# Optimization experiments

Hardware: AMD Instinct MI355X
Metric: run time of the kernel (lower is better)

## Reference

```python
import jax, jax.numpy as jnp
import numpy as np

B, T, N, F = 8, 64, 512, 64
H, FOUT = 128, 64
K = 3          # cheb_k
S = 3          # num_scales
EPS = 1e-8
SPARSITY = 0.3
TEMP = 1.0     # cheb_temp (buffer, temperature == 1.0)


def _xavier(key, fan_out, fan_in, gain):
    limit = gain * np.sqrt(6.0 / (fan_in + fan_out))
    return jax.random.uniform(key, (fan_out, fan_in), jnp.float32, -limit, limit)


def setup_inputs() -> dict:
    key = jax.random.key(0)
    ks = jax.random.split(key, 4)
    x = jax.random.normal(ks[0], (B, T, N, F), jnp.float32)
    # A_param: eye + 0.01*noise, symmetrized (improved_init, N > 64)
    A_param = jnp.eye(N, dtype=jnp.float32) + 0.01 * jax.random.normal(ks[1], (N, N), jnp.float32)
    A_param = 0.5 * (A_param + A_param.T)
    return {
        "x": x,
        "A_param": A_param,
        "alpha_logit": jnp.array(0.0, jnp.float32),  # logit(0.5)
        "in_w": _xavier(ks[2], H, F, np.sqrt(2.0)),
        "in_b": jnp.zeros((H,), jnp.float32),
        "out_w": _xavier(ks[3], FOUT, H, 1.0),
        "out_b": jnp.zeros((FOUT,), jnp.float32),
        "gn_in_w": jnp.ones((F,), jnp.float32), "gn_in_b": jnp.zeros((F,), jnp.float32), "gn_in_ms": jnp.ones((1,), jnp.float32),
        "gn_h_w": jnp.ones((H,), jnp.float32), "gn_h_b": jnp.zeros((H,), jnp.float32), "gn_h_ms": jnp.ones((1,), jnp.float32),
        "gn_out_w": jnp.ones((FOUT,), jnp.float32), "gn_out_b": jnp.zeros((FOUT,), jnp.float32), "gn_out_ms": jnp.ones((1,), jnp.float32),
        "cheb_w": jnp.full((S, K), 1.0 / K, jnp.float32),
        "scale_weights": jnp.full((S,), 1.0 / S, jnp.float32),
    }


def graph_norm(x, w, b, ms, eps=EPS):
    # normalize across the node dim (-2), with learnable mean scale
    mean = x.mean(axis=-2, keepdims=True)
    var = x.var(axis=-2, keepdims=True)  # biased, matches unbiased=False
    xn = (x - mean * ms) * jax.lax.rsqrt(var + eps)
    return xn * w + b


def reference(x, A_param, alpha_logit, in_w, in_b, out_w, out_b,
              gn_in_w, gn_in_b, gn_in_ms, gn_h_w, gn_h_b, gn_h_ms,
              gn_out_w, gn_out_b, gn_out_ms, cheb_w, scale_weights):
    Nv = A_param.shape[0]
    # --- learned graph (training path: tanh + adaptive top-k sparsify) ---
    A = 0.5 * (A_param + A_param.T)
    A = jnp.tanh(A / TEMP)
    k = max(1, int(Nv * (1.0 - SPARSITY)))
    _, idx = jax.lax.top_k(A, k)                       # [N, k] per-row top-k
    mask = jnp.zeros_like(A).at[jnp.arange(Nv)[:, None], idx].set(1.0)
    A_learned = A * mask
    # --- data graph (detached cosine similarity averaged over B*T) ---
    Bv, Tv, Nn, Fv = x.shape
    xt = x.reshape(Bv * Tv, Nn, Fv)
    xt = xt - xt.mean(axis=-1, keepdims=True)
    nrm = jnp.maximum(jnp.linalg.norm(xt, axis=-1, keepdims=True), EPS)
    xn = xt / nrm
    sim = jnp.einsum('bnf,bmf->bnm', xn, xn)
    A_data = jax.lax.stop_gradient(jnp.clip(sim.mean(axis=0), -1.0, 1.0))
    # --- blend ---
    alpha = jax.nn.sigmoid(alpha_logit)
    A_mix = alpha * A_learned + (1.0 - alpha) * A_data
    # --- normalized laplacian, clamped ---
    eye = jnp.eye(Nv, dtype=A_mix.dtype)
    A0 = A_mix * (1.0 - eye)
    deg = A0.sum(axis=-1)
    dinv = jnp.maximum(deg, EPS) ** -0.5
    L = jnp.clip(eye - dinv[:, None] * A0 * dinv[None, :], -1.5, 1.5)
    # --- feature pipeline ---
    xin = graph_norm(x, gn_in_w, gn_in_b, gn_in_ms)
    h = jnp.einsum('btnf,hf->btnh', xin, in_w) + in_b
    # --- multi-scale Chebyshev filter ---
    outs = []
    for s in range(S):
        if s == 0:
            L_s = L
        else:
            Lp = L
            for _ in range(s):
                Lp = Lp @ L
            L_s = jnp.clip(Lp, -1.5, 1.5)
        w = jax.nn.softmax(cheb_w[s] / TEMP)
        T0 = h
        T1 = jnp.einsum('btnf,nm->btmf', h, L_s)
        out = w[0] * T0 + w[1] * T1
        for ki in range(2, K):
            Tk = jnp.clip(2.0 * jnp.einsum('btpf,pm->btmf', T1, L_s) - T0, -50.0, 50.0)
            out = out + w[ki] * Tk
            T0, T1 = T1, Tk
        outs.append(out)
    sw = jax.nn.softmax(scale_weights)
    hc = sum(wv * o for wv, o in zip(sw, outs))
    hh = jax.nn.gelu(graph_norm(hc, gn_h_w, gn_h_b, gn_h_ms))
    y = jnp.einsum('btnh,oh->btno', hh, out_w) + out_b
    return graph_norm(y, gn_out_w, gn_out_b, gn_out_ms)
```

## Files before the change

### kernel.cpp

```cpp
#include <hip/hip_runtime.h>
#include <stdint.h>


typedef unsigned short u16;
using bf16x8 = __attribute__((ext_vector_type(8))) __bf16;
using f32x4  = __attribute__((ext_vector_type(4))) float;

#define DEV __device__ __forceinline__

DEV u16 f2b(float f) {
  union { float f; unsigned u; } v; v.f = f;
  unsigned r = v.u + 0x7FFFu + ((v.u >> 16) & 1u);
  return (u16)(r >> 16);
}
DEV float b2f(u16 b) {
  union { unsigned u; float f; } v; v.u = ((unsigned)b) << 16;
  return v.f;
}
DEV float clampf(float v, float lo, float hi) { return fminf(fmaxf(v, lo), hi); }
DEV bf16x8 pack8(const float* v) {
  union { bf16x8 b; u16 s[8]; } u;
#pragma unroll
  for (int i = 0; i < 8; ++i) u.s[i] = f2b(v[i]);
  return u.b;
}

__global__ __launch_bounds__(256) void k_fill(float* __restrict__ out, float v) {
  out[(size_t)blockIdx.x * 256 + threadIdx.x] = v;
}
__global__ __launch_bounds__(256) void k_zero(float* __restrict__ p) {
  p[(size_t)blockIdx.x * 256 + threadIdx.x] = 0.f;
}

__global__ __launch_bounds__(256) void k_Alearned(const float* __restrict__ Ap,
                                                  float* __restrict__ Aw,
                                                  const float* __restrict__ alpha_l,
                                                  const float* __restrict__ cheb_w,
                                                  const float* __restrict__ scale_w,
                                                  float* __restrict__ scal,
                                                  float* __restrict__ st_out) {
  int i = blockIdx.x;
  if (threadIdx.x < 128) st_out[i * 128 + threadIdx.x] = 0.f;
  __shared__ float row[512];
  for (int j = threadIdx.x; j < 512; j += 256)
    row[j] = tanhf(0.5f * (Ap[i * 512 + j] + Ap[j * 512 + i]));
  __syncthreads();
  for (int j = threadIdx.x; j < 512; j += 256) {
    float v = row[j];
    int rank = 0;
    for (int l = 0; l < 512; ++l) {
      float u = row[l];
      rank += (u > v) || (u == v && l < j);
    }
    Aw[i * 512 + j] = (rank < 358) ? v : 0.f;
  }
  if (i == 0 && threadIdx.x == 0) {
    float alpha = 1.f / (1.f + expf(-alpha_l[0]));
    float sm = fmaxf(fmaxf(scale_w[0], scale_w[1]), scale_w[2]);
    float e0 = expf(scale_w[0] - sm), e1 = expf(scale_w[1] - sm), e2 = expf(scale_w[2] - sm);
    float es = e0 + e1 + e2;
    float sw[3] = { e0 / es, e1 / es, e2 / es };
    float c0 = 0.f, g = 0.f;
    for (int s = 0; s < 3; ++s) {
      float a = cheb_w[s * 3 + 0], b = cheb_w[s * 3 + 1], c = cheb_w[s * 3 + 2];
      float m = fmaxf(fmaxf(a, b), c);
      float f0 = expf(a - m), f1 = expf(b - m), f2 = expf(c - m);
      float fs = f0 + f1 + f2;
      c0 += sw[s] * (f0 / fs);
      scal[2 + s] = sw[s] * (f1 / fs);
      scal[5 + s] = sw[s] * (f2 / fs);
      g += sw[s] * (f2 / fs);
    }
    scal[0] = alpha;
    scal[1] = c0;
    scal[8] = c0 - g;
  }
}

__global__ __launch_bounds__(256) void k_gn_in_stats(const float* __restrict__ x,
                                                     float* __restrict__ st) {
  int bt = blockIdx.x;
  int f = threadIdx.x & 63, seg = threadIdx.x >> 6;
  float s = 0.f, s2 = 0.f;
  for (int n = seg * 128; n < seg * 128 + 128; ++n) {
    float v = x[((size_t)bt * 512 + n) * 64 + f];
    s += v; s2 += v * v;
  }
  __shared__ float ls[4][64], ls2[4][64];
  ls[seg][f] = s; ls2[seg][f] = s2;
  __syncthreads();
  if (seg == 0) {
    float ts = ls[0][f] + ls[1][f] + ls[2][f] + ls[3][f];
    float ts2 = ls2[0][f] + ls2[1][f] + ls2[2][f] + ls2[3][f];
    float mean = ts * (1.f / 512.f);
    float var = fmaxf(ts2 * (1.f / 512.f) - mean * mean, 0.f);
    st[bt * 128 + f * 2] = mean;
    st[bt * 128 + f * 2 + 1] = rsqrtf(var + 1e-8f);
  }
}

__global__ __launch_bounds__(256) void k_xn(const float* __restrict__ x,
                                            u16* __restrict__ Xt) {
  int R = blockIdx.x * 4 + (threadIdx.x >> 6);
  int lane = threadIdx.x & 63;
  int bt = R >> 9, n = R & 511;
  float v = x[(size_t)R * 64 + lane];
  float s = v;
  for (int m = 32; m; m >>= 1) s += __shfl_xor(s, m);
  float c = v - s * (1.f / 64.f);
  float q = c * c;
  for (int m = 32; m; m >>= 1) q += __shfl_xor(q, m);
  float nrm = fmaxf(sqrtf(q), 1e-8f);
  Xt[(size_t)n * 32768 + bt * 64 + lane] = f2b(c / nrm);
}

__global__ __launch_bounds__(256) void k_h(const float* __restrict__ x,
                                           const float* __restrict__ st,
                                           const float* __restrict__ gw,
                                           const float* __restrict__ gb,
                                           const float* __restrict__ msp,
                                           const float* __restrict__ in_w,
                                           const float* __restrict__ in_b,
                                           u16* __restrict__ Hmat) {
  int bt = blockIdx.x >> 1, half = blockIdx.x & 1;
  __shared__ float sc[64], sh[64], bias[128];
  int tid = threadIdx.x;
  float ms = msp[0];
  if (tid < 64) {
    float m = st[bt * 128 + tid * 2], ri = st[bt * 128 + tid * 2 + 1];
    float s = ri * gw[tid];
    sc[tid] = s;
    sh[tid] = gb[tid] - m * ms * s;
  }
  if (tid < 128) bias[tid] = in_b[tid];
  __syncthreads();
  const int lane = tid & 63, w = tid >> 6;
  const int fr = lane & 15, fg = lane >> 4;
  bf16x8 bfrag[8][2];
#pragma unroll
  for (int ni = 0; ni < 8; ++ni)
#pragma unroll
    for (int ks = 0; ks < 2; ++ks) {
      const float* p = in_w + (ni * 16 + fr) * 64 + ks * 32 + fg * 8;
      float4 v0 = *(const float4*)p, v1 = *(const float4*)(p + 4);
      float tmp[8] = { v0.x, v0.y, v0.z, v0.w, v1.x, v1.y, v1.z, v1.w };
      bfrag[ni][ks] = pack8(tmp);
    }
#pragma unroll 1
  for (int mi = 0; mi < 4; ++mi) {
    int n0 = half * 256 + w * 64 + mi * 16;
    bf16x8 af[2];
#pragma unroll
    for (int ks = 0; ks < 2; ++ks) {
      const float* p = x + ((size_t)bt * 512 + n0 + fr) * 64 + ks * 32 + fg * 8;
      float4 v0 = *(const float4*)p, v1 = *(const float4*)(p + 4);
      float raw[8] = { v0.x, v0.y, v0.z, v0.w, v1.x, v1.y, v1.z, v1.w };
      float tmp[8];
#pragma unroll
      for (int j = 0; j < 8; ++j) {
        int f = ks * 32 + fg * 8 + j;
        tmp[j] = raw[j] * sc[f] + sh[f];
      }
      af[ks] = pack8(tmp);
    }
    f32x4 a4[8] = {};
#pragma unroll
    for (int ni = 0; ni < 8; ++ni) {
      a4[ni] = __builtin_amdgcn_mfma_f32_16x16x32_bf16(af[0], bfrag[ni][0], a4[ni], 0, 0, 0);
      a4[ni] = __builtin_amdgcn_mfma_f32_16x16x32_bf16(af[1], bfrag[ni][1], a4[ni], 0, 0, 0);
    }
#pragma unroll
    for (int ni = 0; ni < 8; ++ni) {
      int col = ni * 16 + fr;
      float bi = bias[col];
      union { uint2 u; u16 s[4]; } pk;
#pragma unroll
      for (int r = 0; r < 4; ++r) pk.s[r] = f2b(a4[ni][r] + bi);
      *(uint2*)&Hmat[((size_t)bt * 128 + col) * 512 + n0 + fg * 4] = pk.u;
    }
  }
}

__global__ __launch_bounds__(256) void k_simgemm(const u16* __restrict__ Xt,
                                                 float* __restrict__ Aacc) {
  int tm = (blockIdx.x >> 2) * 128, tn = (blockIdx.x & 3) * 128;
  int kc = blockIdx.y * 2048;
  __shared__ u16 As[128][40], Bs[128][40];
  int tid = threadIdx.x;
  int lane = tid & 63, wave = tid >> 6;
  int wm = (wave >> 1) * 64, wn = (wave & 1) * 64;
  f32x4 accf[4][4] = {};
  const int fr = lane & 15, fk = (lane >> 4) * 8;
  for (int k0 = kc; k0 < kc + 2048; k0 += 32) {
#pragma unroll
    for (int g = 0; g < 2; ++g) {
      int ee = (tid + g * 256) * 8;
      int r = ee >> 5, kk = ee & 31;
      *(uint4*)&As[r][kk] = *(const uint4*)(Xt + (size_t)(tm + r) * 32768 + k0 + kk);
      *(uint4*)&Bs[r][kk] = *(const uint4*)(Xt + (size_t)(tn + r) * 32768 + k0 + kk);
    }
    __syncthreads();
    bf16x8 af[4], bfr[4];
#pragma unroll
    for (int mi = 0; mi < 4; ++mi) af[mi] = *(const bf16x8*)&As[wm + mi * 16 + fr][fk];
#pragma unroll
    for (int ni = 0; ni < 4; ++ni) bfr[ni] = *(const bf16x8*)&Bs[wn + ni * 16 + fr][fk];
#pragma unroll
    for (int mi = 0; mi < 4; ++mi)
#pragma unroll
      for (int ni = 0; ni < 4; ++ni)
        accf[mi][ni] = __builtin_amdgcn_mfma_f32_16x16x32_bf16(af[mi], bfr[ni], accf[mi][ni], 0, 0, 0);
    __syncthreads();
  }
#pragma unroll
  for (int mi = 0; mi < 4; ++mi)
#pragma unroll
    for (int ni = 0; ni < 4; ++ni)
#pragma unroll
      for (int r = 0; r < 4; ++r) {
        int m = tm + wm + mi * 16 + (lane >> 4) * 4 + r;
        int c = tn + wn + ni * 16 + (lane & 15);
        atomicAdd(&Aacc[m * 512 + c], accf[mi][ni][r]);
      }
}

__global__ __launch_bounds__(256) void k_Arow(float* __restrict__ Adacc,
                                              const float* __restrict__ Aw,
                                              const float* __restrict__ scal,
                                              float* __restrict__ deg) {
  int i = blockIdx.x;
  float alpha = scal[0];
  float s = 0.f;
  for (int j = threadIdx.x; j < 512; j += 256) {
    float ad = clampf(Adacc[i * 512 + j] * (1.f / 512.f), -1.f, 1.f);
    float am = alpha * Aw[i * 512 + j] + (1.f - alpha) * ad;
    if (j == i) am = 0.f;
    Adacc[i * 512 + j] = am;
    s += am;
  }
  __shared__ float red[256];
  red[threadIdx.x] = s;
  __syncthreads();
  for (int st_ = 128; st_; st_ >>= 1) {
    if (threadIdx.x < st_) red[threadIdx.x] += red[threadIdx.x + st_];
    __syncthreads();
  }
  if (threadIdx.x == 0) deg[i] = red[0];
}

__global__ __launch_bounds__(256) void k_L(const float* __restrict__ A0,
                                           const float* __restrict__ deg,
                                           float* __restrict__ L) {
  int idx = blockIdx.x * 256 + threadIdx.x;
  int i = idx >> 9, j = idx & 511;
  float di = rsqrtf(fmaxf(deg[i], 1e-8f));
  float dj = rsqrtf(fmaxf(deg[j], 1e-8f));
  float v = ((i == j) ? 1.f : 0.f) - di * A0[idx] * dj;
  L[idx] = clampf(v, -1.5f, 1.5f);
}

__global__ __launch_bounds__(256) void k_mm512c(const float* __restrict__ A,
                                                const float* __restrict__ B,
                                                float* __restrict__ C,
                                                float* __restrict__ Cc) {
  int bi = blockIdx.y, bj = blockIdx.x;
  __shared__ float As[64][65], Bs[64][65];
  int tx = threadIdx.x & 15, ty = threadIdx.x >> 4;
  float acc[4][4] = {};
  for (int k0 = 0; k0 < 512; k0 += 64) {
    for (int e = threadIdx.x; e < 4096; e += 256) {
      int r = e >> 6, c = e & 63;
      As[r][c] = A[(bi * 64 + r) * 512 + k0 + c];
      Bs[r][c] = B[(k0 + r) * 512 + bj * 64 + c];
    }
    __syncthreads();
#pragma unroll 8
    for (int k = 0; k < 64; ++k) {
      float a[4], b[4];
#pragma unroll
      for (int i = 0; i < 4; ++i) { a[i] = As[ty * 4 + i][k]; b[i] = Bs[k][tx * 4 + i]; }
#pragma unroll
      for (int i = 0; i < 4; ++i)
#pragma unroll
        for (int j = 0; j < 4; ++j) acc[i][j] += a[i] * b[j];
    }
    __syncthreads();
  }
#pragma unroll
  for (int i = 0; i < 4; ++i)
#pragma unroll
    for (int j = 0; j < 4; ++j) {
      int idx = (bi * 64 + ty * 4 + i) * 512 + bj * 64 + tx * 4 + j;
      float v = acc[i][j];
      C[idx] = v;
      Cc[idx] = clampf(v, -1.5f, 1.5f);
    }
}

__global__ __launch_bounds__(256) void k_mm512x2(const float* __restrict__ L2c,
                                                 const float* __restrict__ L3c,
                                                 float* __restrict__ Q4,
                                                 float* __restrict__ Q6) {
  const float* A = blockIdx.z ? L3c : L2c;
  float* C = blockIdx.z ? Q6 : Q4;
  int bi = blockIdx.y, bj = blockIdx.x;
  __shared__ float As[64][65], Bs[64][65];
  int tx = threadIdx.x & 15, ty = threadIdx.x >> 4;
  float acc[4][4] = {};
  for (int k0 = 0; k0 < 512; k0 += 64) {
    for (int e = threadIdx.x; e < 4096; e += 256) {
      int r = e >> 6, c = e & 63;
      As[r][c] = A[(bi * 64 + r) * 512 + k0 + c];
      Bs[r][c] = A[(k0 + r) * 512 + bj * 64 + c];
    }
    __syncthreads();
#pragma unroll 8
    for (int k = 0; k < 64; ++k) {
      float a[4], b[4];
#pragma unroll
      for (int i = 0; i < 4; ++i) { a[i] = As[ty * 4 + i][k]; b[i] = Bs[k][tx * 4 + i]; }
#pragma unroll
      for (int i = 0; i < 4; ++i)
#pragma unroll
        for (int j = 0; j < 4; ++j) acc[i][j] += a[i] * b[j];
    }
    __syncthreads();
  }
#pragma unroll
  for (int i = 0; i < 4; ++i)
#pragma unroll
    for (int j = 0; j < 4; ++j)
      C[(bi * 64 + ty * 4 + i) * 512 + bj * 64 + tx * 4 + j] = acc[i][j];
}

__global__ __launch_bounds__(256) void k_qcombine(const float* __restrict__ L,
                                                  const float* __restrict__ L2c,
                                                  const float* __restrict__ L3c,
                                                  const float* __restrict__ P2,
                                                  const float* __restrict__ Q4,
                                                  const float* __restrict__ Q6,
                                                  const float* __restrict__ scal,
                                                  u16* __restrict__ QTb) {
  __shared__ u16 t[64][65];
  int i0 = (blockIdx.x >> 3) * 64, j0 = (blockIdx.x & 7) * 64;
  float a1 = scal[2], a2 = scal[3], a3 = scal[4];
  float b1 = 2.f * scal[5], b2 = 2.f * scal[6], b3 = 2.f * scal[7];
  float g = scal[8];
  for (int e = threadIdx.x; e < 4096; e += 256) {
    int r = e >> 6, c = e & 63;
    int idx = (i0 + r) * 512 + j0 + c;
    float q = a1 * L[idx] + a2 * L2c[idx] + a3 * L3c[idx]
            + b1 * P2[idx] + b2 * Q4[idx] + b3 * Q6[idx];
    if (i0 + r == j0 + c) q += g;
    t[c][r] = f2b(q);
  }
  __syncthreads();
  for (int e = threadIdx.x; e < 4096; e += 256) {
    int r = e >> 6, c = e & 63;
    QTb[(j0 + r) * 512 + i0 + c] = t[r][c];
  }
}

__global__ __launch_bounds__(512, 4) void k_hcq3(const u16* __restrict__ Hg,
                                                 const u16* __restrict__ QT,
                                                 u16* __restrict__ accB,
                                                 int cbase,
                                                 float* __restrict__ st_h) {
  __shared__ u16 Hs[64][512];
  __shared__ float sS[64][8], sS2[64][8];
  const int tid = threadIdx.x;
  const int lane = tid & 63, w = tid >> 6;
  const int fr = lane & 15, hi = lane >> 4;
  const int cblk = blockIdx.x * 64;
  const int wn = w * 64;
  for (int e = tid; e < 4096; e += 512) {
    int r = e >> 6, kk = (e & 63) * 8;
    *(uint4*)&Hs[r][kk ^ ((r & 7) << 3)] =
        *(const uint4*)(Hg + (size_t)(cblk + r) * 512 + kk);
  }
  __syncthreads();
  const int csw = (fr & 7) << 3;
  f32x4 acc[4][4] = {};
#pragma unroll 1
  for (int k0 = 0; k0 < 512; k0 += 32) {
    bf16x8 af[4], bf[4];
#pragma unroll
    for (int ci = 0; ci < 4; ++ci)
      af[ci] = *(const bf16x8*)&Hs[ci * 16 + fr][(k0 + hi * 8) ^ csw];
#pragma unroll
    for (int ni = 0; ni < 4; ++ni)
      bf[ni] = *(const bf16x8*)(QT + (size_t)(wn + ni * 16 + fr) * 512 + k0 + hi * 8);
#pragma unroll
    for (int ni = 0; ni < 4; ++ni)
#pragma unroll
      for (int ci = 0; ci < 4; ++ci)
        acc[ni][ci] = __builtin_amdgcn_mfma_f32_16x16x32_bf16(bf[ni], af[ci], acc[ni][ci], 0, 0, 0);
  }
#pragma unroll
  for (int ci = 0; ci < 4; ++ci) {
    float a = 0.f, b = 0.f;
#pragma unroll
    for (int ni = 0; ni < 4; ++ni)
#pragma unroll
      for (int r = 0; r < 4; ++r) {
        float v = acc[ni][ci][r];
        a += v; b += v * v;
      }
    a += __shfl_xor(a, 16); a += __shfl_xor(a, 32);
    b += __shfl_xor(b, 16); b += __shfl_xor(b, 32);
    if (hi == 0) { sS[ci * 16 + fr][w] = a; sS2[ci * 16 + fr][w] = b; }
  }
  __syncthreads();
  if (tid < 64) {
    float a = 0.f, b = 0.f;
#pragma unroll
    for (int ww = 0; ww < 8; ++ww) { a += sS[tid][ww]; b += sS2[tid][ww]; }
    float mean = a * (1.f / 512.f);
    float var = fmaxf(b * (1.f / 512.f) - mean * mean, 0.f);
    int cg = cbase + cblk + tid;
    int bt = cg >> 7, h = cg & 127;
    st_h[bt * 256 + h * 2] = mean;
    st_h[bt * 256 + h * 2 + 1] = rsqrtf(var + 1e-8f);
  }
#pragma unroll
  for (int ni = 0; ni < 4; ++ni)
#pragma unroll
    for (int ci = 0; ci < 4; ++ci) {
      union { uint2 u; u16 s4[4]; } pk;
#pragma unroll
      for (int r = 0; r < 4; ++r) pk.s4[r] = f2b(acc[ni][ci][r]);
      *(uint2*)&accB[(size_t)(cblk + ci * 16 + fr) * 512 + wn + ni * 16 + hi * 4] = pk.u;
    }
}

__global__ __launch_bounds__(256) void k_y(const u16* __restrict__ acc_c,
                                           int btbase,
                                           const float* __restrict__ st,
                                           const float* __restrict__ gw,
                                           const float* __restrict__ gb,
                                           const float* __restrict__ msp,
                                           const float* __restrict__ out_w,
                                           const float* __restrict__ out_b,
                                           float* __restrict__ dout,
                                           float* __restrict__ st_out) {
  int btl = blockIdx.x >> 2, q = blockIdx.x & 3;
  int bt = btbase + btl;
  __shared__ u16 G[128][136];
  __shared__ float sc[128], sh[128], bias[64];
  __shared__ float sY[64][4], sQv[64][4];
  int tid = threadIdx.x;
  float ms = msp[0];
  if (tid < 128) {
    float m = st[bt * 256 + tid * 2], ri = st[bt * 256 + tid * 2 + 1];
    float s = ri * gw[tid];
    sc[tid] = s;
    sh[tid] = gb[tid] - m * ms * s;
  }
  if (tid < 64) bias[tid] = out_b[tid];
  const int lane = tid & 63, w = tid >> 6;
  const int fr = lane & 15, fg = lane >> 4;
  bf16x8 bfrag[4][4];
#pragma unroll
  for (int ni = 0; ni < 4; ++ni)
#pragma unroll
    for (int ks = 0; ks < 4; ++ks) {
      const float* p = out_w + (ni * 16 + fr) * 128 + ks * 32 + fg * 8;
      float4 v0 = *(const float4*)p, v1 = *(const float4*)(p + 4);
      float tmp[8] = { v0.x, v0.y, v0.z, v0.w, v1.x, v1.y, v1.z, v1.w };
      bfrag[ni][ks] = pack8(tmp);
    }
  __syncthreads();
  {
    int h = tid >> 1, nh = (tid & 1) * 64;
    float scv = sc[h], shv = sh[h];
    const u16* src = acc_c + ((size_t)btl * 128 + h) * 512 + q * 128 + nh;
#pragma unroll
    for (int j = 0; j < 8; ++j) {
      uint4 v = *(const uint4*)(src + j * 8);
      const u16* pv = (const u16*)&v;
#pragma unroll
      for (int i = 0; i < 8; ++i) {
        float xg = b2f(pv[i]) * scv + shv;
        float y = 0.79788456f * (xg + 0.044715f * xg * xg * xg);
        float g = xg / (1.f + __expf(-2.f * y));
        G[nh + j * 8 + i][h] = f2b(g);
      }
    }
  }
  __syncthreads();
  float so[4] = { 0.f, 0.f, 0.f, 0.f }, sq[4] = { 0.f, 0.f, 0.f, 0.f };
#pragma unroll
  for (int mi = 0; mi < 2; ++mi) {
    int nloc = w * 32 + mi * 16;
    bf16x8 af[4];
#pragma unroll
    for (int ks = 0; ks < 4; ++ks)
      af[ks] = *(const bf16x8*)&G[nloc + fr][ks * 32 + fg * 8];
    f32x4 a4[4] = {};
#pragma unroll
    for (int ni = 0; ni < 4; ++ni)
#pragma unroll
      for (int ks = 0; ks < 4; ++ks)
        a4[ni] = __builtin_amdgcn_mfma_f32_16x16x32_bf16(af[ks], bfrag[ni][ks], a4[ni], 0, 0, 0);
#pragma unroll
    for (int ni = 0; ni < 4; ++ni) {
      int o = ni * 16 + fr;
      float bi = bias[o];
#pragma unroll
      for (int r = 0; r < 4; ++r) {
        float yv = a4[ni][r] + bi;
        so[ni] += yv; sq[ni] += yv * yv;
        dout[((size_t)bt * 512 + q * 128 + nloc + fg * 4 + r) * 64 + o] = yv;
      }
    }
  }
#pragma unroll
  for (int ni = 0; ni < 4; ++ni) {
    float a = so[ni], b = sq[ni];
    a += __shfl_xor(a, 16); a += __shfl_xor(a, 32);
    b += __shfl_xor(b, 16); b += __shfl_xor(b, 32);
    if (fg == 0) { sY[ni * 16 + fr][w] = a; sQv[ni * 16 + fr][w] = b; }
  }
  __syncthreads();
  if (tid < 64) {
    float a = sY[tid][0] + sY[tid][1] + sY[tid][2] + sY[tid][3];
    float b = sQv[tid][0] + sQv[tid][1] + sQv[tid][2] + sQv[tid][3];
    atomicAdd(&st_out[bt * 128 + tid * 2], a);
    atomicAdd(&st_out[bt * 128 + tid * 2 + 1], b);
  }
}

__global__ __launch_bounds__(256) void k_outf2(float* __restrict__ ybuf,
                                               const float* __restrict__ S,
                                               const float* __restrict__ gw,
                                               const float* __restrict__ gb,
                                               const float* __restrict__ msp) {
  float ms = msp[0];
  for (int idx = blockIdx.x * 256 + threadIdx.x; idx < 16777216; idx += 8192 * 256) {
    int bt = idx >> 15;
    int o = idx & 63;
    float sum = S[bt * 128 + o * 2], ssq = S[bt * 128 + o * 2 + 1];
    float mean = sum * (1.f / 512.f);
    float var = fmaxf(ssq * (1.f / 512.f) - mean * mean, 0.f);
    float v = ybuf[idx];
    ybuf[idx] = (v - mean * ms) * rsqrtf(var + 1e-8f) * gw[o] + gb[o];
  }
}

extern "C" void kernel_launch(void* const* d_in, const int* in_sizes, int n_in,
                              void* d_out, int out_size, void* d_ws, size_t ws_size,
                              hipStream_t stream) {
  (void)in_sizes; (void)n_in; (void)out_size;
  const float* x        = (const float*)d_in[0];
  const float* A_param  = (const float*)d_in[1];
  const float* alpha_l  = (const float*)d_in[2];
  const float* in_w     = (const float*)d_in[3];
  const float* in_b     = (const float*)d_in[4];
  const float* out_w    = (const float*)d_in[5];
  const float* out_b    = (const float*)d_in[6];
  const float* gn_in_w  = (const float*)d_in[7];
  const float* gn_in_b  = (const float*)d_in[8];
  const float* gn_in_ms = (const float*)d_in[9];
  const float* gn_h_w   = (const float*)d_in[10];
  const float* gn_h_b   = (const float*)d_in[11];
  const float* gn_h_ms  = (const float*)d_in[12];
  const float* gn_out_w = (const float*)d_in[13];
  const float* gn_out_b = (const float*)d_in[14];
  const float* gn_out_ms= (const float*)d_in[15];
  const float* cheb_w   = (const float*)d_in[16];
  const float* scale_w  = (const float*)d_in[17];
  float* out = (float*)d_out;

  char* ws = (char*)d_ws;
  float* A_work = (float*)(ws + (0ull << 20));
  float* A_dacc = (float*)(ws + (1ull << 20));
  float* Lbuf   = (float*)(ws + (2ull << 20));
  float* P2raw  = (float*)(ws + (3ull << 20));
  float* P3raw  = (float*)(ws + (4ull << 20));
  float* L2c    = (float*)(ws + (5ull << 20));
  float* L3c    = (float*)(ws + (6ull << 20));
  float* Q4     = (float*)(ws + (0ull << 20));
  float* Q6     = (float*)(ws + (1ull << 20));
  u16*   QTb    = (u16*)(ws + (7ull << 20));
  float* deg    = (float*)(ws + (7ull << 20) + 524288);
  float* scal   = (float*)(ws + (7ull << 20) + 524288 + 4096);
  float* st_in  = (float*)(ws + (8ull << 20));
  float* st_h   = (float*)(ws + (8ull << 20) + 262144);
  float* st_out = (float*)(ws + (8ull << 20) + 262144 + 524288);
  u16*   Hmat   = (u16*)(ws + (10ull << 20));
  char*  chunkbase = ws + (74ull << 20);
  u16*   Xt     = (u16*)chunkbase;
  u16*   accB   = (u16*)chunkbase;

  const size_t baseNeed = 74ull << 20;
  int NC;
  if      (ws_size >= baseNeed + (64ull << 20)) NC = 1;
  else if (ws_size >= baseNeed + (32ull << 20)) NC = 2;
  else {
    k_fill<<<65536, 256, 0, stream>>>(out, (float)(ws_size >> 20));
    return;
  }
  const int CC = 65536 / NC;
  const int NBT = CC / 128;

  k_Alearned<<<512, 256, 0, stream>>>(A_param, A_work, alpha_l, cheb_w, scale_w,
                                      scal, st_out);
  k_gn_in_stats<<<512, 256, 0, stream>>>(x, st_in);
  k_xn<<<65536, 256, 0, stream>>>(x, Xt);
  k_h<<<1024, 256, 0, stream>>>(x, st_in, gn_in_w, gn_in_b, gn_in_ms, in_w, in_b, Hmat);
  k_zero<<<1024, 256, 0, stream>>>(A_dacc);
  k_simgemm<<<dim3(16, 16), 256, 0, stream>>>(Xt, A_dacc);
  k_Arow<<<512, 256, 0, stream>>>(A_dacc, A_work, scal, deg);
  k_L<<<1024, 256, 0, stream>>>(A_dacc, deg, Lbuf);
  k_mm512c<<<dim3(8, 8), 256, 0, stream>>>(Lbuf, Lbuf, P2raw, L2c);
  k_mm512c<<<dim3(8, 8), 256, 0, stream>>>(P2raw, Lbuf, P3raw, L3c);
  k_mm512x2<<<dim3(8, 8, 2), 256, 0, stream>>>(L2c, L3c, Q4, Q6);
  k_qcombine<<<64, 256, 0, stream>>>(Lbuf, L2c, L3c, P2raw, Q4, Q6, scal, QTb);

  for (int ch = 0; ch < NC; ++ch) {
    const int cbase = ch * CC;
    const int btbase = ch * NBT;
    k_hcq3<<<CC / 64, 512, 0, stream>>>(Hmat + (size_t)cbase * 512, QTb, accB,
                                        cbase, st_h);
    k_y<<<NBT * 4, 256, 0, stream>>>(accB, btbase, st_h, gn_h_w, gn_h_b, gn_h_ms,
                                     out_w, out_b, out, st_out);
  }

  k_outf2<<<8192, 256, 0, stream>>>(out, st_out, gn_out_w, gn_out_b, gn_out_ms);
}
```

Before: 546.6 us.

## Fuse small kernels, shrink 512x512 matmul tiles, relax hcq3 launch bounds

```diff
diff --git a/kernel.cpp b/kernel.cpp
--- a/kernel.cpp
+++ b/kernel.cpp
@@ -27,9 +27,6 @@
 
 __global__ __launch_bounds__(256) void k_fill(float* __restrict__ out, float v) {
   out[(size_t)blockIdx.x * 256 + threadIdx.x] = v;
-}
-__global__ __launch_bounds__(256) void k_zero(float* __restrict__ p) {
-  p[(size_t)blockIdx.x * 256 + threadIdx.x] = 0.f;
 }
 
 __global__ __launch_bounds__(256) void k_Alearned(const float* __restrict__ Ap,
@@ -38,9 +35,12 @@
                                                   const float* __restrict__ cheb_w,
                                                   const float* __restrict__ scale_w,
                                                   float* __restrict__ scal,
-                                                  float* __restrict__ st_out) {
+                                                  float* __restrict__ st_out,
+                                                  float* __restrict__ Adacc) {
   int i = blockIdx.x;
   if (threadIdx.x < 128) st_out[i * 128 + threadIdx.x] = 0.f;
+  Adacc[i * 512 + threadIdx.x] = 0.f;
+  Adacc[i * 512 + 256 + threadIdx.x] = 0.f;
   __shared__ float row[512];
   for (int j = threadIdx.x; j < 512; j += 256)
     row[j] = tanhf(0.5f * (Ap[i * 512 + j] + Ap[j * 512 + i]));
@@ -77,41 +77,43 @@
   }
 }
 
-__global__ __launch_bounds__(256) void k_gn_in_stats(const float* __restrict__ x,
-                                                     float* __restrict__ st) {
+__global__ __launch_bounds__(256) void k_gnxn(const float* __restrict__ x,
+                                              float* __restrict__ st,
+                                              u16* __restrict__ Xt) {
   int bt = blockIdx.x;
-  int f = threadIdx.x & 63, seg = threadIdx.x >> 6;
-  float s = 0.f, s2 = 0.f;
-  for (int n = seg * 128; n < seg * 128 + 128; ++n) {
-    float v = x[((size_t)bt * 512 + n) * 64 + f];
-    s += v; s2 += v * v;
-  }
-  __shared__ float ls[4][64], ls2[4][64];
-  ls[seg][f] = s; ls2[seg][f] = s2;
-  __syncthreads();
-  if (seg == 0) {
-    float ts = ls[0][f] + ls[1][f] + ls[2][f] + ls[3][f];
-    float ts2 = ls2[0][f] + ls2[1][f] + ls2[2][f] + ls2[3][f];
-    float mean = ts * (1.f / 512.f);
-    float var = fmaxf(ts2 * (1.f / 512.f) - mean * mean, 0.f);
-    st[bt * 128 + f * 2] = mean;
-    st[bt * 128 + f * 2 + 1] = rsqrtf(var + 1e-8f);
-  }
-}
-
-__global__ __launch_bounds__(256) void k_xn(const float* __restrict__ x,
-                                            u16* __restrict__ Xt) {
-  int R = blockIdx.x * 4 + (threadIdx.x >> 6);
-  int lane = threadIdx.x & 63;
-  int bt = R >> 9, n = R & 511;
-  float v = x[(size_t)R * 64 + lane];
-  float s = v;
-  for (int m = 32; m; m >>= 1) s += __shfl_xor(s, m);
-  float c = v - s * (1.f / 64.f);
-  float q = c * c;
-  for (int m = 32; m; m >>= 1) q += __shfl_xor(q, m);
-  float nrm = fmaxf(sqrtf(q), 1e-8f);
-  Xt[(size_t)n * 32768 + bt * 64 + lane] = f2b(c / nrm);
+  int tid = threadIdx.x;
+  {
+    int f = tid & 63, seg = tid >> 6;
+    float s = 0.f, s2 = 0.f;
+    for (int n = seg * 128; n < seg * 128 + 128; ++n) {
+      float v = x[((size_t)bt * 512 + n) * 64 + f];
+      s += v; s2 += v * v;
+    }
+    __shared__ float ls[4][64], ls2[4][64];
+    ls[seg][f] = s; ls2[seg][f] = s2;
+    __syncthreads();
+    if (seg == 0) {
+      float ts = ls[0][f] + ls[1][f] + ls[2][f] + ls[3][f];
+      float ts2 = ls2[0][f] + ls2[1][f] + ls2[2][f] + ls2[3][f];
+      float mean = ts * (1.f / 512.f);
+      float var = fmaxf(ts2 * (1.f / 512.f) - mean * mean, 0.f);
+      st[bt * 128 + f * 2] = mean;
+      st[bt * 128 + f * 2 + 1] = rsqrtf(var + 1e-8f);
+    }
+  }
+  {
+    int lane = tid & 63, w = tid >> 6;
+    for (int n = w; n < 512; n += 4) {
+      float v = x[((size_t)bt * 512 + n) * 64 + lane];
+      float s = v;
+      for (int m = 32; m; m >>= 1) s += __shfl_xor(s, m);
+      float c = v - s * (1.f / 64.f);
+      float q = c * c;
+      for (int m = 32; m; m >>= 1) q += __shfl_xor(q, m);
+      float nrm = fmaxf(sqrtf(q), 1e-8f);
+      Xt[(size_t)n * 32768 + bt * 64 + lane] = f2b(c / nrm);
+    }
+  }
 }
 
 __global__ __launch_bounds__(256) void k_h(const float* __restrict__ x,
@@ -264,33 +266,33 @@
                                                 float* __restrict__ C,
                                                 float* __restrict__ Cc) {
   int bi = blockIdx.y, bj = blockIdx.x;
-  __shared__ float As[64][65], Bs[64][65];
+  __shared__ float As[32][65], Bs[64][33];
   int tx = threadIdx.x & 15, ty = threadIdx.x >> 4;
-  float acc[4][4] = {};
+  float acc[2][2] = {};
   for (int k0 = 0; k0 < 512; k0 += 64) {
-    for (int e = threadIdx.x; e < 4096; e += 256) {
+    for (int e = threadIdx.x; e < 2048; e += 256) {
       int r = e >> 6, c = e & 63;
-      As[r][c] = A[(bi * 64 + r) * 512 + k0 + c];
-      Bs[r][c] = B[(k0 + r) * 512 + bj * 64 + c];
+      As[r][c] = A[(bi * 32 + r) * 512 + k0 + c];
+    }
+    for (int e = threadIdx.x; e < 2048; e += 256) {
+      int r = e >> 5, c = e & 31;
+      Bs[r][c] = B[(k0 + r) * 512 + bj * 32 + c];
     }
     __syncthreads();
 #pragma unroll 8
     for (int k = 0; k < 64; ++k) {
-      float a[4], b[4];
-#pragma unroll
-      for (int i = 0; i < 4; ++i) { a[i] = As[ty * 4 + i][k]; b[i] = Bs[k][tx * 4 + i]; }
-#pragma unroll
-      for (int i = 0; i < 4; ++i)
-#pragma unroll
-        for (int j = 0; j < 4; ++j) acc[i][j] += a[i] * b[j];
-    }
-    __syncthreads();
-  }
-#pragma unroll
-  for (int i = 0; i < 4; ++i)
-#pragma unroll
-    for (int j = 0; j < 4; ++j) {
-      int idx = (bi * 64 + ty * 4 + i) * 512 + bj * 64 + tx * 4 + j;
+      float a0 = As[ty * 2][k], a1 = As[ty * 2 + 1][k];
+      float b0 = Bs[k][tx * 2], b1 = Bs[k][tx * 2 + 1];
+      acc[0][0] += a0 * b0; acc[0][1] += a0 * b1;
+      acc[1][0] += a1 * b0; acc[1][1] += a1 * b1;
+    }
+    __syncthreads();
+  }
+#pragma unroll
+  for (int i = 0; i < 2; ++i)
+#pragma unroll
+    for (int j = 0; j < 2; ++j) {
+      int idx = (bi * 32 + ty * 2 + i) * 512 + bj * 32 + tx * 2 + j;
       float v = acc[i][j];
       C[idx] = v;
       Cc[idx] = clampf(v, -1.5f, 1.5f);
@@ -304,33 +306,33 @@
   const float* A = blockIdx.z ? L3c : L2c;
   float* C = blockIdx.z ? Q6 : Q4;
   int bi = blockIdx.y, bj = blockIdx.x;
-  __shared__ float As[64][65], Bs[64][65];
+  __shared__ float As[32][65], Bs[64][33];
   int tx = threadIdx.x & 15, ty = threadIdx.x >> 4;
-  float acc[4][4] = {};
+  float acc[2][2] = {};
   for (int k0 = 0; k0 < 512; k0 += 64) {
-    for (int e = threadIdx.x; e < 4096; e += 256) {
+    for (int e = threadIdx.x; e < 2048; e += 256) {
       int r = e >> 6, c = e & 63;
-      As[r][c] = A[(bi * 64 + r) * 512 + k0 + c];
-      Bs[r][c] = A[(k0 + r) * 512 + bj * 64 + c];
+      As[r][c] = A[(bi * 32 + r) * 512 + k0 + c];
+    }
+    for (int e = threadIdx.x; e < 2048; e += 256) {
+      int r = e >> 5, c = e & 31;
+      Bs[r][c] = A[(k0 + r) * 512 + bj * 32 + c];
     }
     __syncthreads();
 #pragma unroll 8
     for (int k = 0; k < 64; ++k) {
-      float a[4], b[4];
-#pragma unroll
-      for (int i = 0; i < 4; ++i) { a[i] = As[ty * 4 + i][k]; b[i] = Bs[k][tx * 4 + i]; }
-#pragma unroll
-      for (int i = 0; i < 4; ++i)
-#pragma unroll
-        for (int j = 0; j < 4; ++j) acc[i][j] += a[i] * b[j];
-    }
-    __syncthreads();
-  }
-#pragma unroll
-  for (int i = 0; i < 4; ++i)
-#pragma unroll
-    for (int j = 0; j < 4; ++j)
-      C[(bi * 64 + ty * 4 + i) * 512 + bj * 64 + tx * 4 + j] = acc[i][j];
+      float a0 = As[ty * 2][k], a1 = As[ty * 2 + 1][k];
+      float b0 = Bs[k][tx * 2], b1 = Bs[k][tx * 2 + 1];
+      acc[0][0] += a0 * b0; acc[0][1] += a0 * b1;
+      acc[1][0] += a1 * b0; acc[1][1] += a1 * b1;
+    }
+    __syncthreads();
+  }
+#pragma unroll
+  for (int i = 0; i < 2; ++i)
+#pragma unroll
+    for (int j = 0; j < 2; ++j)
+      C[(bi * 32 + ty * 2 + i) * 512 + bj * 32 + tx * 2 + j] = acc[i][j];
 }
 
 __global__ __launch_bounds__(256) void k_qcombine(const float* __restrict__ L,
@@ -361,7 +363,7 @@
   }
 }
 
-__global__ __launch_bounds__(512, 4) void k_hcq3(const u16* __restrict__ Hg,
+__global__ __launch_bounds__(512, 2) void k_hcq3(const u16* __restrict__ Hg,
                                                  const u16* __restrict__ QT,
                                                  u16* __restrict__ accB,
                                                  int cbase,
@@ -381,7 +383,7 @@
   __syncthreads();
   const int csw = (fr & 7) << 3;
   f32x4 acc[4][4] = {};
-#pragma unroll 1
+#pragma unroll 2
   for (int k0 = 0; k0 < 512; k0 += 32) {
     bf16x8 af[4], bf[4];
 #pragma unroll
@@ -604,17 +606,15 @@
   const int NBT = CC / 128;
 
   k_Alearned<<<512, 256, 0, stream>>>(A_param, A_work, alpha_l, cheb_w, scale_w,
-                                      scal, st_out);
-  k_gn_in_stats<<<512, 256, 0, stream>>>(x, st_in);
-  k_xn<<<65536, 256, 0, stream>>>(x, Xt);
+                                      scal, st_out, A_dacc);
+  k_gnxn<<<512, 256, 0, stream>>>(x, st_in, Xt);
   k_h<<<1024, 256, 0, stream>>>(x, st_in, gn_in_w, gn_in_b, gn_in_ms, in_w, in_b, Hmat);
-  k_zero<<<1024, 256, 0, stream>>>(A_dacc);
   k_simgemm<<<dim3(16, 16), 256, 0, stream>>>(Xt, A_dacc);
   k_Arow<<<512, 256, 0, stream>>>(A_dacc, A_work, scal, deg);
   k_L<<<1024, 256, 0, stream>>>(A_dacc, deg, Lbuf);
-  k_mm512c<<<dim3(8, 8), 256, 0, stream>>>(Lbuf, Lbuf, P2raw, L2c);
-  k_mm512c<<<dim3(8, 8), 256, 0, stream>>>(P2raw, Lbuf, P3raw, L3c);
-  k_mm512x2<<<dim3(8, 8, 2), 256, 0, stream>>>(L2c, L3c, Q4, Q6);
+  k_mm512c<<<dim3(16, 16), 256, 0, stream>>>(Lbuf, Lbuf, P2raw, L2c);
+  k_mm512c<<<dim3(16, 16), 256, 0, stream>>>(P2raw, Lbuf, P3raw, L3c);
+  k_mm512x2<<<dim3(16, 16, 2), 256, 0, stream>>>(L2c, L3c, Q4, Q6);
   k_qcombine<<<64, 256, 0, stream>>>(Lbuf, L2c, L3c, P2raw, Q4, Q6, scal, QTb);
 
   for (int ch = 0; ch < NC; ++ch) {
```

After: 528.2 us. 1.03x faster.
